# Kernel tuning notes

Measured on AMD Instinct MI355X. Metric: run time of the kernel, lower is better.

## Reference

```python
import jax, jax.numpy as jnp
import numpy as np

B, T, D, H = 4, 2048, 1024, 16
Dh = D // H          # 64 head dim
NF = Dh // 2         # 32 rotary frequencies


def setup_inputs() -> dict:
    key = jax.random.key(0)
    k0, k1, k2, k3 = jax.random.split(key, 4)
    x = jax.random.normal(k0, (B, T, D), dtype=jnp.float32)
    # 3D spatial coordinates per token, e.g. voxel positions
    coords = jax.random.uniform(k1, (B, T, 3), dtype=jnp.float32, minval=0.0, maxval=64.0)
    w_scale = 1.0 / np.sqrt(D)
    qkv_w = jax.random.normal(k2, (3 * D, D), dtype=jnp.float32) * w_scale
    qkv_b = jnp.zeros((3 * D,), dtype=jnp.float32)
    proj_w = jax.random.normal(k3, (D, D), dtype=jnp.float32) * w_scale
    proj_b = jnp.zeros((D,), dtype=jnp.float32)
    # mixed-axis rope: frequency f uses coordinate axis (f % 3), geometric period spacing within each axis group
    axes = (jnp.arange(NF) % 3).astype(jnp.int32)
    group = (jnp.arange(NF) // 3).astype(jnp.float32)
    n_per_axis = float(NF) / 3.0
    inv_freq = (10000.0 ** (-group / n_per_axis)).astype(jnp.float32)
    return {"x": x, "coords": coords, "qkv_w": qkv_w, "qkv_b": qkv_b,
            "proj_w": proj_w, "proj_b": proj_b, "inv_freq": inv_freq, "axes": axes}


def _apply_rope(t, sin, cos):
    # t: [B, H, T, Dh]; sin/cos: [B, 1, T, Dh//2]  (rotate-half convention)
    t1, t2 = jnp.split(t, 2, axis=-1)
    return jnp.concatenate([t1 * cos - t2 * sin, t1 * sin + t2 * cos], axis=-1)


def reference(x, coords, qkv_w, qkv_b, proj_w, proj_b, inv_freq, axes):
    b, t, d = x.shape
    # fused QKV projection
    qkv = (x @ qkv_w.T + qkv_b).reshape(b, t, 3, H, Dh)
    qkv = jnp.transpose(qkv, (2, 0, 3, 1, 4))     # [3, B, H, T, Dh]
    q, k, v = qkv[0], qkv[1], qkv[2]
    # vectorized per-sample rope from coords (replaces python loop over batch)
    ang = jnp.take(coords, axes, axis=-1) * inv_freq      # [B, T, NF]
    sin = jnp.sin(ang)[:, None]                            # [B, 1, T, NF]
    cos = jnp.cos(ang)[:, None]
    q = _apply_rope(q, sin, cos)
    k = _apply_rope(k, sin, cos)
    # standard scaling mode: single 1/sqrt(Dh) inside SDPA
    scale = 1.0 / np.sqrt(Dh)
    scores = jnp.einsum('bhqd,bhkd->bhqk', q, k) * scale
    attn = jax.nn.softmax(scores, axis=-1)
    out = jnp.einsum('bhqk,bhkd->bhqd', attn, v)           # [B, H, T, Dh]
    out = jnp.transpose(out, (0, 2, 1, 3)).reshape(b, t, d)
    return out @ proj_w.T + proj_b
```

## Files before the change

kernel.cpp:

```cpp
#include <hip/hip_runtime.h>
#include <hip/hip_bf16.h>

#define B_ 4
#define T_ 2048
#define D_ 1024
#define H_ 16
#define DH 64
#define NF 32
#define BH (B_*H_)
#define M_ROWS (B_*T_)

#define QSCALE 0.125f

using u16 = unsigned short;
using u32 = unsigned int;

typedef __bf16 bf16x8 __attribute__((ext_vector_type(8)));
typedef float  f32x4  __attribute__((ext_vector_type(4)));
typedef float  f32x16 __attribute__((ext_vector_type(16)));

__device__ __forceinline__ u16 f2bf(float f) {
  u32 u = __float_as_uint(f);
  u32 r = u + 0x7fffu + ((u >> 16) & 1u);
  return (u16)(r >> 16);
}
__device__ __forceinline__ u16 f2bf_hw(float f) {
  __bf16 h = (__bf16)f;
  return *(u16*)&h;
}
__device__ __forceinline__ u32 pack2(float lo, float hi) {
  return (u32)f2bf_hw(lo) | ((u32)f2bf_hw(hi) << 16);
}
__device__ __forceinline__ float bf2f(u16 h) {
  return __uint_as_float(((u32)h) << 16);
}

__device__ __forceinline__ void pl32swap(u32 a, u32 b, u32& x, u32& y) {
  x = a; y = b;
  asm("s_nop 1\n\t"
      "v_permlane32_swap_b32 %0, %1"
      : "+v"(x), "+v"(y));
}

__device__ __forceinline__ void gload_lds16(const void* g, void* l) {
  __builtin_amdgcn_global_load_lds((__attribute__((address_space(1))) void*)(g),
                                   (__attribute__((address_space(3))) void*)(l),
                                   16, 0, 0);
}

__global__ __launch_bounds__(256)
void cvt_kernel(const float* __restrict__ in, u16* __restrict__ out, int n8) {
  int idx = blockIdx.x * 256 + threadIdx.x;
  if (idx >= n8) return;
  const float4* p = (const float4*)in + (long)idx * 2;
  float4 a = p[0], b = p[1];
  u32 o0 = (u32)f2bf(a.x) | ((u32)f2bf(a.y) << 16);
  u32 o1 = (u32)f2bf(a.z) | ((u32)f2bf(a.w) << 16);
  u32 o2 = (u32)f2bf(b.x) | ((u32)f2bf(b.y) << 16);
  u32 o3 = (u32)f2bf(b.z) | ((u32)f2bf(b.w) << 16);
  ((uint4*)out)[idx] = make_uint4(o0, o1, o2, o3);
}

__global__ __launch_bounds__(256)
void sincos_kernel(const float* __restrict__ coords, const float* __restrict__ inv_freq,
                   const int* __restrict__ axes, float* __restrict__ sc) {
  int idx = blockIdx.x * 256 + threadIdx.x;
  if (idx >= B_ * T_ * NF) return;
  int f = idx & 31;
  long bt = idx >> 5;
  float c = coords[bt * 3 + axes[f]];
  float ang = c * inv_freq[f];
  sc[bt * 64 + f]      = sinf(ang);
  sc[bt * 64 + 32 + f] = cosf(ang);
}

__global__ __launch_bounds__(256, 2)
void gemm_qkv(const u16* __restrict__ A, const u16* __restrict__ Bt,
              const float* __restrict__ bias, const float* __restrict__ sc,
              u16* __restrict__ qr, u16* __restrict__ kr, u16* __restrict__ vt) {
  const int N = 3 * D_, K = D_;
  __shared__ u16 SMEM[128 * 64 * 2];
  u16* As = SMEM;
  u16* Bs = SMEM + 128 * 64;
  int nb = N >> 7;
  int bid = blockIdx.x;
  int nwg = gridDim.x;
  int cpx = nwg >> 3;
  bid = (bid & 7) * cpx + (bid >> 3);
  int bm = bid / nb, bn = bid % nb;
  long m0 = (long)bm << 7, n0 = (long)bn << 7;
  int tid = threadIdx.x;
  int lane = tid & 63, w = tid >> 6;
  int g = lane >> 4, lr = lane & 15;
  int wm = w >> 1, wn = w & 1;

  f32x4 acc[4][4] = {};

  for (int kt = 0; kt < K; kt += 64) {
    __syncthreads();
    #pragma unroll
    for (int j = 0; j < 4; ++j) {
      int ob = j * 4096 + tid * 16;
      int row = ob >> 7, col = (ob & 127) >> 1;
      u16* ldsA = As + j * 2048 + w * 512;
      u16* ldsB = Bs + j * 2048 + w * 512;
      gload_lds16(A + (m0 + row) * K + kt + col, ldsA);
      gload_lds16(Bt + (n0 + row) * K + kt + col, ldsB);
    }
    __syncthreads();
    #pragma unroll
    for (int kk = 0; kk < 2; ++kk) {
      bf16x8 af[4], bfr[4];
      #pragma unroll
      for (int i = 0; i < 4; ++i)
        af[i] = *(const bf16x8*)(As + (wm * 64 + i * 16 + lr) * 64 + kk * 32 + g * 8);
      #pragma unroll
      for (int i = 0; i < 4; ++i)
        bfr[i] = *(const bf16x8*)(Bs + (wn * 64 + i * 16 + lr) * 64 + kk * 32 + g * 8);
      #pragma unroll
      for (int mi = 0; mi < 4; ++mi)
        #pragma unroll
        for (int nj = 0; nj < 4; ++nj)
          acc[mi][nj] = __builtin_amdgcn_mfma_f32_16x16x32_bf16(af[mi], bfr[nj], acc[mi][nj], 0, 0, 0);
    }
  }

  int part = (int)(n0 >> 10);
  int b = (int)(m0 >> 11), t0 = (int)(m0 & 2047);
  float bv[4];
  #pragma unroll
  for (int nj = 0; nj < 4; ++nj)
    bv[nj] = bias[n0 + wn * 64 + nj * 16 + lr];

  if (part == 2) {
    int h0 = (int)((n0 & 1023) >> 6);
    u16* Vsm = SMEM;
    #pragma unroll
    for (int hsel = 0; hsel < 2; ++hsel) {
      __syncthreads();
      if (wn == hsel) {
        #pragma unroll
        for (int mi = 0; mi < 4; ++mi)
          #pragma unroll
          for (int i = 0; i < 4; ++i) {
            int lrow = wm * 64 + mi * 16 + g * 4 + i;
            #pragma unroll
            for (int nj = 0; nj < 4; ++nj)
              Vsm[lrow * 72 + nj * 16 + lr] = f2bf(acc[mi][nj][i] + bv[nj]);
          }
      }
      __syncthreads();
      int d = tid >> 2, tc = tid & 3;
      long obase = ((long)((b * 16 + h0 + hsel) * DH + d)) * T_ + t0 + tc * 32;
      #pragma unroll
      for (int c = 0; c < 4; ++c) {
        u32 o[4];
        #pragma unroll
        for (int j = 0; j < 4; ++j) {
          u16 lo = Vsm[(tc * 32 + c * 8 + 2 * j)     * 72 + d];
          u16 hi = Vsm[(tc * 32 + c * 8 + 2 * j + 1) * 72 + d];
          o[j] = (u32)lo | ((u32)hi << 16);
        }
        *(uint4*)(vt + obase + c * 8) = make_uint4(o[0], o[1], o[2], o[3]);
      }
    }
  } else {
    int h = ((int)(n0 & 1023) >> 6) + wn;
    u16* outp = part ? kr : qr;
    float fac = part ? 1.0f : QSCALE;
    #pragma unroll
    for (int mi = 0; mi < 4; ++mi) {
      #pragma unroll
      for (int i = 0; i < 4; ++i) {
        long row = m0 + wm * 64 + mi * 16 + g * 4 + i;
        long obase = ((long)((b * 16 + h)) * T_ + (row & 2047)) * 64;
        const float* scp = sc + row * 64;
        #pragma unroll
        for (int nj = 0; nj < 2; ++nj) {
          int d = nj * 16 + lr;
          float sn = scp[d], cs = scp[32 + d];
          float t1 = acc[mi][nj][i]     + bv[nj];
          float t2 = acc[mi][nj + 2][i] + bv[nj + 2];
          outp[obase + d]      = f2bf((t1 * cs - t2 * sn) * fac);
          outp[obase + 32 + d] = f2bf((t1 * sn + t2 * cs) * fac);
        }
      }
    }
  }
}

__global__ __launch_bounds__(256, 2)
void gemm_bt(const u16* __restrict__ A, const u16* __restrict__ Bt,
             const float* __restrict__ bias, float* __restrict__ Cout,
             int M, int N, int K) {
  __shared__ u16 As[128 * 64];
  __shared__ u16 Bs[128 * 64];
  int nb = N >> 7;
  int bid = blockIdx.x;
  int nwg = gridDim.x;
  if ((nwg & 7) == 0) {
    int c = nwg >> 3;
    bid = (bid & 7) * c + (bid >> 3);
  }
  int bm = bid / nb, bn = bid % nb;
  long m0 = (long)bm << 7, n0 = (long)bn << 7;
  int tid = threadIdx.x;
  int lane = tid & 63, w = tid >> 6;
  int g = lane >> 4, lr = lane & 15;
  int wm = w >> 1, wn = w & 1;

  f32x4 acc[4][4] = {};

  for (int kt = 0; kt < K; kt += 64) {
    __syncthreads();
    #pragma unroll
    for (int j = 0; j < 4; ++j) {
      int ob = j * 4096 + tid * 16;
      int row = ob >> 7, col = (ob & 127) >> 1;
      u16* ldsA = As + j * 2048 + w * 512;
      u16* ldsB = Bs + j * 2048 + w * 512;
      gload_lds16(A + (m0 + row) * K + kt + col, ldsA);
      gload_lds16(Bt + (n0 + row) * K + kt + col, ldsB);
    }
    __syncthreads();
    #pragma unroll
    for (int kk = 0; kk < 2; ++kk) {
      bf16x8 af[4], bfr[4];
      #pragma unroll
      for (int i = 0; i < 4; ++i)
        af[i] = *(const bf16x8*)(As + (wm * 64 + i * 16 + lr) * 64 + kk * 32 + g * 8);
      #pragma unroll
      for (int i = 0; i < 4; ++i)
        bfr[i] = *(const bf16x8*)(Bs + (wn * 64 + i * 16 + lr) * 64 + kk * 32 + g * 8);
      #pragma unroll
      for (int mi = 0; mi < 4; ++mi)
        #pragma unroll
        for (int nj = 0; nj < 4; ++nj)
          acc[mi][nj] = __builtin_amdgcn_mfma_f32_16x16x32_bf16(af[mi], bfr[nj], acc[mi][nj], 0, 0, 0);
    }
  }
  #pragma unroll
  for (int mi = 0; mi < 4; ++mi) {
    #pragma unroll
    for (int nj = 0; nj < 4; ++nj) {
      long col = n0 + wn * 64 + nj * 16 + lr;
      float bvv = bias[col];
      #pragma unroll
      for (int i = 0; i < 4; ++i) {
        long row = m0 + wm * 64 + mi * 16 + g * 4 + i;
        Cout[row * (long)N + col] = acc[mi][nj][i] + bvv;
      }
    }
  }
}

__global__ __launch_bounds__(256, 2)
void attn_kernel(const u16* __restrict__ Qr, const u16* __restrict__ Kr,
                 const u16* __restrict__ Vt, u16* __restrict__ Aout) {
  __shared__ u16 Ks[2][2][64 * 64];
  __shared__ u16 Vs[2][2][64 * 64];
  int wg = (blockIdx.x & 7) * 64 + (blockIdx.x >> 3);
  int bh = wg >> 3;
  int b = bh >> 4, h = bh & 15;
  int q0 = (wg & 7) << 8;
  int tid = threadIdx.x;
  int lane = tid & 63, w = tid >> 6;
  int l5 = lane & 31, hb = lane >> 5;

  const long tbase = (long)bh * T_;
  const long vbase = (long)bh * DH;
  const int qs = q0 + w * 64;

  bf16x8 bq0[4], bq1[4];
  #pragma unroll
  for (int s = 0; s < 4; ++s) {
    bq0[s] = *(const bf16x8*)(Qr + (tbase + qs + l5)      * DH + s * 16 + hb * 8);
    bq1[s] = *(const bf16x8*)(Qr + (tbase + qs + 32 + l5) * DH + s * 16 + hb * 8);
  }

  f32x16 oa00 = {}, oa01 = {};
  f32x16 oa10 = {}, oa11 = {};
  float ls0 = 0.f, ls1 = 0.f;

  const int sl = l5 & 7;

  auto STAGE = [&](int buf, int kb) {
    #pragma unroll
    for (int sub = 0; sub < 2; ++sub) {
      #pragma unroll
      for (int j = 0; j < 2; ++j) {
        int ob = j * 4096 + tid * 16;
        int row = ob >> 7;
        int c = ((ob >> 4) & 7) ^ (row & 7);
        u16* ldsK = Ks[buf][sub] + j * 2048 + w * 512;
        u16* ldsV = Vs[buf][sub] + j * 2048 + w * 512;
        gload_lds16(Kr + (tbase + kb + sub * 64 + row) * DH + c * 8, ldsK);
        gload_lds16(Vt + (vbase + row) * T_ + kb + sub * 64 + c * 8, ldsV);
      }
    }
  };

  STAGE(0, 0);
  asm volatile("s_waitcnt vmcnt(0)" ::: "memory");
  __builtin_amdgcn_s_barrier();
  __builtin_amdgcn_sched_barrier(0);

  int cur = 0;
  for (int kt = 0; kt < T_ / 128; ++kt) {
    if (kt + 1 < T_ / 128) STAGE(cur ^ 1, (kt + 1) * 128);

    #pragma unroll
    for (int h2 = 0; h2 < 2; ++h2) {
      const u16* kbuf = Ks[cur][h2];
      const u16* vbuf = Vs[cur][h2];

      f32x16 p00 = {}, p01 = {}, p10 = {}, p11 = {};
      #pragma unroll
      for (int s = 0; s < 4; ++s) {
        int c = ((2 * s + hb) ^ sl) * 8;
        bf16x8 ak0 = *(const bf16x8*)(kbuf + l5 * 64 + c);
        bf16x8 ak1 = *(const bf16x8*)(kbuf + (32 + l5) * 64 + c);
        p00 = __builtin_amdgcn_mfma_f32_32x32x16_bf16(ak0, bq0[s], p00, 0, 0, 0);
        p01 = __builtin_amdgcn_mfma_f32_32x32x16_bf16(ak1, bq0[s], p01, 0, 0, 0);
        p10 = __builtin_amdgcn_mfma_f32_32x32x16_bf16(ak0, bq1[s], p10, 0, 0, 0);
        p11 = __builtin_amdgcn_mfma_f32_32x32x16_bf16(ak1, bq1[s], p11, 0, 0, 0);
      }

      u32 pA0[8], pB0[8], pA1[8], pB1[8];
      #pragma unroll
      for (int r4 = 0; r4 < 4; ++r4) {
        float a0 = __expf(p00[4 * r4 + 0]), a1 = __expf(p00[4 * r4 + 1]);
        float a2 = __expf(p00[4 * r4 + 2]), a3 = __expf(p00[4 * r4 + 3]);
        ls0 += (a0 + a1) + (a2 + a3);
        pA0[r4] = pack2(a0, a1); pB0[r4] = pack2(a2, a3);
        float b0 = __expf(p01[4 * r4 + 0]), b1 = __expf(p01[4 * r4 + 1]);
        float b2 = __expf(p01[4 * r4 + 2]), b3 = __expf(p01[4 * r4 + 3]);
        ls0 += (b0 + b1) + (b2 + b3);
        pA0[4 + r4] = pack2(b0, b1); pB0[4 + r4] = pack2(b2, b3);
        float c0 = __expf(p10[4 * r4 + 0]), c1 = __expf(p10[4 * r4 + 1]);
        float c2 = __expf(p10[4 * r4 + 2]), c3 = __expf(p10[4 * r4 + 3]);
        ls1 += (c0 + c1) + (c2 + c3);
        pA1[r4] = pack2(c0, c1); pB1[r4] = pack2(c2, c3);
        float d0 = __expf(p11[4 * r4 + 0]), d1 = __expf(p11[4 * r4 + 1]);
        float d2 = __expf(p11[4 * r4 + 2]), d3 = __expf(p11[4 * r4 + 3]);
        ls1 += (d0 + d1) + (d2 + d3);
        pA1[4 + r4] = pack2(d0, d1); pB1[4 + r4] = pack2(d2, d3);
      }

      #pragma unroll
      for (int s2 = 0; s2 < 4; ++s2) {
        int c = ((2 * s2 + hb) ^ sl) * 8;
        bf16x8 av0 = *(const bf16x8*)(vbuf + l5 * 64 + c);
        bf16x8 av1 = *(const bf16x8*)(vbuf + (32 + l5) * 64 + c);
        u32 w0, w1, w2, w3;
        pl32swap(pA0[2 * s2], pA0[2 * s2 + 1], w0, w2);
        pl32swap(pB0[2 * s2], pB0[2 * s2 + 1], w1, w3);
        union { u32 u[4]; bf16x8 v; } bw0;
        bw0.u[0] = w0; bw0.u[1] = w1; bw0.u[2] = w2; bw0.u[3] = w3;
        oa00 = __builtin_amdgcn_mfma_f32_32x32x16_bf16(av0, bw0.v, oa00, 0, 0, 0);
        oa01 = __builtin_amdgcn_mfma_f32_32x32x16_bf16(av1, bw0.v, oa01, 0, 0, 0);
        pl32swap(pA1[2 * s2], pA1[2 * s2 + 1], w0, w2);
        pl32swap(pB1[2 * s2], pB1[2 * s2 + 1], w1, w3);
        union { u32 u[4]; bf16x8 v; } bw1;
        bw1.u[0] = w0; bw1.u[1] = w1; bw1.u[2] = w2; bw1.u[3] = w3;
        oa10 = __builtin_amdgcn_mfma_f32_32x32x16_bf16(av0, bw1.v, oa10, 0, 0, 0);
        oa11 = __builtin_amdgcn_mfma_f32_32x32x16_bf16(av1, bw1.v, oa11, 0, 0, 0);
      }
    }

    __builtin_amdgcn_sched_barrier(0);
    asm volatile("s_waitcnt vmcnt(0)" ::: "memory");
    __builtin_amdgcn_s_barrier();
    __builtin_amdgcn_sched_barrier(0);
    cur ^= 1;
  }

  ls0 += __shfl_xor(ls0, 32);
  ls1 += __shfl_xor(ls1, 32);
  float inv0 = 1.0f / ls0;
  float inv1 = 1.0f / ls1;
  long row0 = (long)b * T_ + qs + l5;
  u16* ob0 = Aout + row0 * D_ + h * DH;
  u16* ob1 = ob0 + 32 * D_;
  #pragma unroll
  for (int r4 = 0; r4 < 4; ++r4) {
    u32 w0 = pack2(oa00[4 * r4 + 0] * inv0, oa00[4 * r4 + 1] * inv0);
    u32 w1 = pack2(oa00[4 * r4 + 2] * inv0, oa00[4 * r4 + 3] * inv0);
    *(uint2*)(ob0 + r4 * 8 + hb * 4) = make_uint2(w0, w1);
    u32 w2 = pack2(oa01[4 * r4 + 0] * inv0, oa01[4 * r4 + 1] * inv0);
    u32 w3 = pack2(oa01[4 * r4 + 2] * inv0, oa01[4 * r4 + 3] * inv0);
    *(uint2*)(ob0 + 32 + r4 * 8 + hb * 4) = make_uint2(w2, w3);
    u32 w4 = pack2(oa10[4 * r4 + 0] * inv1, oa10[4 * r4 + 1] * inv1);
    u32 w5 = pack2(oa10[4 * r4 + 2] * inv1, oa10[4 * r4 + 3] * inv1);
    *(uint2*)(ob1 + r4 * 8 + hb * 4) = make_uint2(w4, w5);
    u32 w6 = pack2(oa11[4 * r4 + 0] * inv1, oa11[4 * r4 + 1] * inv1);
    u32 w7 = pack2(oa11[4 * r4 + 2] * inv1, oa11[4 * r4 + 3] * inv1);
    *(uint2*)(ob1 + 32 + r4 * 8 + hb * 4) = make_uint2(w6, w7);
  }
}

extern "C" void kernel_launch(void* const* d_in, const int* in_sizes, int n_in,
                              void* d_out, int out_size, void* d_ws, size_t ws_size,
                              hipStream_t stream) {
  const float* x        = (const float*)d_in[0];
  const float* coords   = (const float*)d_in[1];
  const float* qkv_w    = (const float*)d_in[2];
  const float* qkv_b    = (const float*)d_in[3];
  const float* proj_w   = (const float*)d_in[4];
  const float* proj_b   = (const float*)d_in[5];
  const float* inv_freq = (const float*)d_in[6];
  const int*   axes     = (const int*)d_in[7];
  float* out = (float*)d_out;

  char* ws = (char*)d_ws;
  size_t off = 0;
  auto alloc = [&](size_t bytes) -> char* {
    char* p = ws + off;
    off += (bytes + 255) & ~(size_t)255;
    return p;
  };
  u16*   xb     = (u16*)  alloc((size_t)M_ROWS * D_ * 2);
  u16*   wqkv   = (u16*)  alloc((size_t)3 * D_ * D_ * 2);
  u16*   wproj  = (u16*)  alloc((size_t)D_ * D_ * 2);
  float* sc     = (float*)alloc((size_t)M_ROWS * 64 * 4);
  u16*   qr     = (u16*)  alloc((size_t)BH * T_ * DH * 2);
  u16*   kr     = (u16*)  alloc((size_t)BH * T_ * DH * 2);
  u16*   vt     = (u16*)  alloc((size_t)BH * T_ * DH * 2);
  u16*   aout   = (u16*)  alloc((size_t)BH * T_ * DH * 2);

  cvt_kernel<<<(M_ROWS * D_ / 8 + 255) / 256, 256, 0, stream>>>(x, xb, M_ROWS * D_ / 8);
  cvt_kernel<<<(3 * D_ * D_ / 8 + 255) / 256, 256, 0, stream>>>(qkv_w, wqkv, 3 * D_ * D_ / 8);
  cvt_kernel<<<(D_ * D_ / 8 + 255) / 256, 256, 0, stream>>>(proj_w, wproj, D_ * D_ / 8);
  sincos_kernel<<<(B_ * T_ * NF + 255) / 256, 256, 0, stream>>>(coords, inv_freq, axes, sc);

  gemm_qkv<<<(M_ROWS / 128) * (3 * D_ / 128), 256, 0, stream>>>(xb, wqkv, qkv_b, sc,
                                                                qr, kr, vt);
  attn_kernel<<<512, 256, 0, stream>>>(qr, kr, vt, aout);
  gemm_bt<<<(M_ROWS / 128) * (D_ / 128), 256, 0, stream>>>(aout, wproj, proj_b, out,
                                                           M_ROWS, D_, D_);
}
```

Measured before the change: 203.8 us.

## Split attention KV range across two workgroups and merge partials in combine kernel

```diff
diff --git a/kernel.cpp b/kernel.cpp
--- a/kernel.cpp
+++ b/kernel.cpp
@@ -48,11 +48,9 @@
                                    16, 0, 0);
 }
 
-__global__ __launch_bounds__(256)
-void cvt_kernel(const float* __restrict__ in, u16* __restrict__ out, int n8) {
-  int idx = blockIdx.x * 256 + threadIdx.x;
-  if (idx >= n8) return;
-  const float4* p = (const float4*)in + (long)idx * 2;
+__device__ __forceinline__ void cvt8(const float* __restrict__ in,
+                                     u16* __restrict__ out, long idx) {
+  const float4* p = (const float4*)in + idx * 2;
   float4 a = p[0], b = p[1];
   u32 o0 = (u32)f2bf(a.x) | ((u32)f2bf(a.y) << 16);
   u32 o1 = (u32)f2bf(a.z) | ((u32)f2bf(a.w) << 16);
@@ -62,16 +60,31 @@
 }
 
 __global__ __launch_bounds__(256)
-void sincos_kernel(const float* __restrict__ coords, const float* __restrict__ inv_freq,
-                   const int* __restrict__ axes, float* __restrict__ sc) {
-  int idx = blockIdx.x * 256 + threadIdx.x;
-  if (idx >= B_ * T_ * NF) return;
-  int f = idx & 31;
-  long bt = idx >> 5;
-  float c = coords[bt * 3 + axes[f]];
-  float ang = c * inv_freq[f];
-  sc[bt * 64 + f]      = sinf(ang);
-  sc[bt * 64 + 32 + f] = cosf(ang);
+void prep_kernel(const float* __restrict__ x, u16* __restrict__ xb,
+                 const float* __restrict__ qkv_w, u16* __restrict__ wqkv,
+                 const float* __restrict__ proj_w, u16* __restrict__ wproj,
+                 const float* __restrict__ coords, const float* __restrict__ inv_freq,
+                 const int* __restrict__ axes, float* __restrict__ sc) {
+  long idx = (long)blockIdx.x * 256 + threadIdx.x;
+  const long n1 = (long)M_ROWS * D_ / 8;
+  const long n2 = n1 + 3L * D_ * D_ / 8;
+  const long n3 = n2 + (long)D_ * D_ / 8;
+  const long n4 = n3 + (long)B_ * T_ * NF;
+  if (idx < n1) {
+    cvt8(x, xb, idx);
+  } else if (idx < n2) {
+    cvt8(qkv_w, wqkv, idx - n1);
+  } else if (idx < n3) {
+    cvt8(proj_w, wproj, idx - n2);
+  } else if (idx < n4) {
+    long j = idx - n3;
+    int f = (int)(j & 31);
+    long bt = j >> 5;
+    float c = coords[bt * 3 + axes[f]];
+    float ang = c * inv_freq[f];
+    sc[bt * 64 + f]      = sinf(ang);
+    sc[bt * 64 + 32 + f] = cosf(ang);
+  }
 }
 
 __global__ __launch_bounds__(256, 2)
@@ -254,15 +267,19 @@
   }
 }
 
-__global__ __launch_bounds__(256, 2)
+__global__ __launch_bounds__(256, 4)
 void attn_kernel(const u16* __restrict__ Qr, const u16* __restrict__ Kr,
-                 const u16* __restrict__ Vt, u16* __restrict__ Aout) {
-  __shared__ u16 Ks[2][2][64 * 64];
-  __shared__ u16 Vs[2][2][64 * 64];
-  int wg = (blockIdx.x & 7) * 64 + (blockIdx.x >> 3);
-  int bh = wg >> 3;
+                 const u16* __restrict__ Vt, u16* __restrict__ P,
+                 float* __restrict__ L) {
+  __shared__ u16 Ks[2][64 * 64];
+  __shared__ u16 Vs[2][64 * 64];
+  int wg = (blockIdx.x & 7) * 128 + (blockIdx.x >> 3);
+  int bh = wg >> 4;
+  int sub = wg & 15;
+  int q0 = (sub >> 1) << 8;
+  int kv = sub & 1;
+  int kb0 = kv << 10;
   int b = bh >> 4, h = bh & 15;
-  int q0 = (wg & 7) << 8;
   int tid = threadIdx.x;
   int lane = tid & 63, w = tid >> 6;
   int l5 = lane & 31, hb = lane >> 5;
@@ -286,86 +303,80 @@
 
   auto STAGE = [&](int buf, int kb) {
     #pragma unroll
-    for (int sub = 0; sub < 2; ++sub) {
-      #pragma unroll
-      for (int j = 0; j < 2; ++j) {
-        int ob = j * 4096 + tid * 16;
-        int row = ob >> 7;
-        int c = ((ob >> 4) & 7) ^ (row & 7);
-        u16* ldsK = Ks[buf][sub] + j * 2048 + w * 512;
-        u16* ldsV = Vs[buf][sub] + j * 2048 + w * 512;
-        gload_lds16(Kr + (tbase + kb + sub * 64 + row) * DH + c * 8, ldsK);
-        gload_lds16(Vt + (vbase + row) * T_ + kb + sub * 64 + c * 8, ldsV);
-      }
+    for (int j = 0; j < 2; ++j) {
+      int ob = j * 4096 + tid * 16;
+      int row = ob >> 7;
+      int c = ((ob >> 4) & 7) ^ (row & 7);
+      u16* ldsK = Ks[buf] + j * 2048 + w * 512;
+      u16* ldsV = Vs[buf] + j * 2048 + w * 512;
+      gload_lds16(Kr + (tbase + kb + row) * DH + c * 8, ldsK);
+      gload_lds16(Vt + (vbase + row) * T_ + kb + c * 8, ldsV);
     }
   };
 
-  STAGE(0, 0);
+  STAGE(0, kb0);
   asm volatile("s_waitcnt vmcnt(0)" ::: "memory");
   __builtin_amdgcn_s_barrier();
   __builtin_amdgcn_sched_barrier(0);
 
   int cur = 0;
-  for (int kt = 0; kt < T_ / 128; ++kt) {
-    if (kt + 1 < T_ / 128) STAGE(cur ^ 1, (kt + 1) * 128);
-
-    #pragma unroll
-    for (int h2 = 0; h2 < 2; ++h2) {
-      const u16* kbuf = Ks[cur][h2];
-      const u16* vbuf = Vs[cur][h2];
-
-      f32x16 p00 = {}, p01 = {}, p10 = {}, p11 = {};
-      #pragma unroll
-      for (int s = 0; s < 4; ++s) {
-        int c = ((2 * s + hb) ^ sl) * 8;
-        bf16x8 ak0 = *(const bf16x8*)(kbuf + l5 * 64 + c);
-        bf16x8 ak1 = *(const bf16x8*)(kbuf + (32 + l5) * 64 + c);
-        p00 = __builtin_amdgcn_mfma_f32_32x32x16_bf16(ak0, bq0[s], p00, 0, 0, 0);
-        p01 = __builtin_amdgcn_mfma_f32_32x32x16_bf16(ak1, bq0[s], p01, 0, 0, 0);
-        p10 = __builtin_amdgcn_mfma_f32_32x32x16_bf16(ak0, bq1[s], p10, 0, 0, 0);
-        p11 = __builtin_amdgcn_mfma_f32_32x32x16_bf16(ak1, bq1[s], p11, 0, 0, 0);
-      }
-
-      u32 pA0[8], pB0[8], pA1[8], pB1[8];
-      #pragma unroll
-      for (int r4 = 0; r4 < 4; ++r4) {
-        float a0 = __expf(p00[4 * r4 + 0]), a1 = __expf(p00[4 * r4 + 1]);
-        float a2 = __expf(p00[4 * r4 + 2]), a3 = __expf(p00[4 * r4 + 3]);
-        ls0 += (a0 + a1) + (a2 + a3);
-        pA0[r4] = pack2(a0, a1); pB0[r4] = pack2(a2, a3);
-        float b0 = __expf(p01[4 * r4 + 0]), b1 = __expf(p01[4 * r4 + 1]);
-        float b2 = __expf(p01[4 * r4 + 2]), b3 = __expf(p01[4 * r4 + 3]);
-        ls0 += (b0 + b1) + (b2 + b3);
-        pA0[4 + r4] = pack2(b0, b1); pB0[4 + r4] = pack2(b2, b3);
-        float c0 = __expf(p10[4 * r4 + 0]), c1 = __expf(p10[4 * r4 + 1]);
-        float c2 = __expf(p10[4 * r4 + 2]), c3 = __expf(p10[4 * r4 + 3]);
-        ls1 += (c0 + c1) + (c2 + c3);
-        pA1[r4] = pack2(c0, c1); pB1[r4] = pack2(c2, c3);
-        float d0 = __expf(p11[4 * r4 + 0]), d1 = __expf(p11[4 * r4 + 1]);
-        float d2 = __expf(p11[4 * r4 + 2]), d3 = __expf(p11[4 * r4 + 3]);
-        ls1 += (d0 + d1) + (d2 + d3);
-        pA1[4 + r4] = pack2(d0, d1); pB1[4 + r4] = pack2(d2, d3);
-      }
-
-      #pragma unroll
-      for (int s2 = 0; s2 < 4; ++s2) {
-        int c = ((2 * s2 + hb) ^ sl) * 8;
-        bf16x8 av0 = *(const bf16x8*)(vbuf + l5 * 64 + c);
-        bf16x8 av1 = *(const bf16x8*)(vbuf + (32 + l5) * 64 + c);
-        u32 w0, w1, w2, w3;
-        pl32swap(pA0[2 * s2], pA0[2 * s2 + 1], w0, w2);
-        pl32swap(pB0[2 * s2], pB0[2 * s2 + 1], w1, w3);
-        union { u32 u[4]; bf16x8 v; } bw0;
-        bw0.u[0] = w0; bw0.u[1] = w1; bw0.u[2] = w2; bw0.u[3] = w3;
-        oa00 = __builtin_amdgcn_mfma_f32_32x32x16_bf16(av0, bw0.v, oa00, 0, 0, 0);
-        oa01 = __builtin_amdgcn_mfma_f32_32x32x16_bf16(av1, bw0.v, oa01, 0, 0, 0);
-        pl32swap(pA1[2 * s2], pA1[2 * s2 + 1], w0, w2);
-        pl32swap(pB1[2 * s2], pB1[2 * s2 + 1], w1, w3);
-        union { u32 u[4]; bf16x8 v; } bw1;
-        bw1.u[0] = w0; bw1.u[1] = w1; bw1.u[2] = w2; bw1.u[3] = w3;
-        oa10 = __builtin_amdgcn_mfma_f32_32x32x16_bf16(av0, bw1.v, oa10, 0, 0, 0);
-        oa11 = __builtin_amdgcn_mfma_f32_32x32x16_bf16(av1, bw1.v, oa11, 0, 0, 0);
-      }
+  for (int kt = 0; kt < 16; ++kt) {
+    if (kt + 1 < 16) STAGE(cur ^ 1, kb0 + (kt + 1) * 64);
+
+    const u16* kbuf = Ks[cur];
+    const u16* vbuf = Vs[cur];
+
+    f32x16 p00 = {}, p01 = {}, p10 = {}, p11 = {};
+    #pragma unroll
+    for (int s = 0; s < 4; ++s) {
+      int c = ((2 * s + hb) ^ sl) * 8;
+      bf16x8 ak0 = *(const bf16x8*)(kbuf + l5 * 64 + c);
+      bf16x8 ak1 = *(const bf16x8*)(kbuf + (32 + l5) * 64 + c);
+      p00 = __builtin_amdgcn_mfma_f32_32x32x16_bf16(ak0, bq0[s], p00, 0, 0, 0);
+      p01 = __builtin_amdgcn_mfma_f32_32x32x16_bf16(ak1, bq0[s], p01, 0, 0, 0);
+      p10 = __builtin_amdgcn_mfma_f32_32x32x16_bf16(ak0, bq1[s], p10, 0, 0, 0);
+      p11 = __builtin_amdgcn_mfma_f32_32x32x16_bf16(ak1, bq1[s], p11, 0, 0, 0);
+    }
+
+    u32 pA0[8], pB0[8], pA1[8], pB1[8];
+    #pragma unroll
+    for (int r4 = 0; r4 < 4; ++r4) {
+      float a0 = __expf(p00[4 * r4 + 0]), a1 = __expf(p00[4 * r4 + 1]);
+      float a2 = __expf(p00[4 * r4 + 2]), a3 = __expf(p00[4 * r4 + 3]);
+      ls0 += (a0 + a1) + (a2 + a3);
+      pA0[r4] = pack2(a0, a1); pB0[r4] = pack2(a2, a3);
+      float b0 = __expf(p01[4 * r4 + 0]), b1 = __expf(p01[4 * r4 + 1]);
+      float b2 = __expf(p01[4 * r4 + 2]), b3 = __expf(p01[4 * r4 + 3]);
+      ls0 += (b0 + b1) + (b2 + b3);
+      pA0[4 + r4] = pack2(b0, b1); pB0[4 + r4] = pack2(b2, b3);
+      float c0 = __expf(p10[4 * r4 + 0]), c1 = __expf(p10[4 * r4 + 1]);
+      float c2 = __expf(p10[4 * r4 + 2]), c3 = __expf(p10[4 * r4 + 3]);
+      ls1 += (c0 + c1) + (c2 + c3);
+      pA1[r4] = pack2(c0, c1); pB1[r4] = pack2(c2, c3);
+      float d0 = __expf(p11[4 * r4 + 0]), d1 = __expf(p11[4 * r4 + 1]);
+      float d2 = __expf(p11[4 * r4 + 2]), d3 = __expf(p11[4 * r4 + 3]);
+      ls1 += (d0 + d1) + (d2 + d3);
+      pA1[4 + r4] = pack2(d0, d1); pB1[4 + r4] = pack2(d2, d3);
+    }
+
+    #pragma unroll
+    for (int s2 = 0; s2 < 4; ++s2) {
+      int c = ((2 * s2 + hb) ^ sl) * 8;
+      bf16x8 av0 = *(const bf16x8*)(vbuf + l5 * 64 + c);
+      bf16x8 av1 = *(const bf16x8*)(vbuf + (32 + l5) * 64 + c);
+      u32 w0, w1, w2, w3;
+      pl32swap(pA0[2 * s2], pA0[2 * s2 + 1], w0, w2);
+      pl32swap(pB0[2 * s2], pB0[2 * s2 + 1], w1, w3);
+      union { u32 u[4]; bf16x8 v; } bw0;
+      bw0.u[0] = w0; bw0.u[1] = w1; bw0.u[2] = w2; bw0.u[3] = w3;
+      oa00 = __builtin_amdgcn_mfma_f32_32x32x16_bf16(av0, bw0.v, oa00, 0, 0, 0);
+      oa01 = __builtin_amdgcn_mfma_f32_32x32x16_bf16(av1, bw0.v, oa01, 0, 0, 0);
+      pl32swap(pA1[2 * s2], pA1[2 * s2 + 1], w0, w2);
+      pl32swap(pB1[2 * s2], pB1[2 * s2 + 1], w1, w3);
+      union { u32 u[4]; bf16x8 v; } bw1;
+      bw1.u[0] = w0; bw1.u[1] = w1; bw1.u[2] = w2; bw1.u[3] = w3;
+      oa10 = __builtin_amdgcn_mfma_f32_32x32x16_bf16(av0, bw1.v, oa10, 0, 0, 0);
+      oa11 = __builtin_amdgcn_mfma_f32_32x32x16_bf16(av1, bw1.v, oa11, 0, 0, 0);
     }
 
     __builtin_amdgcn_sched_barrier(0);
@@ -377,26 +388,59 @@
 
   ls0 += __shfl_xor(ls0, 32);
   ls1 += __shfl_xor(ls1, 32);
-  float inv0 = 1.0f / ls0;
-  float inv1 = 1.0f / ls1;
+  const long PS = (long)BH * T_ * DH;
+  u16* Pout = P + (long)kv * PS;
   long row0 = (long)b * T_ + qs + l5;
-  u16* ob0 = Aout + row0 * D_ + h * DH;
+  u16* ob0 = Pout + row0 * D_ + h * DH;
   u16* ob1 = ob0 + 32 * D_;
   #pragma unroll
   for (int r4 = 0; r4 < 4; ++r4) {
-    u32 w0 = pack2(oa00[4 * r4 + 0] * inv0, oa00[4 * r4 + 1] * inv0);
-    u32 w1 = pack2(oa00[4 * r4 + 2] * inv0, oa00[4 * r4 + 3] * inv0);
+    u32 w0 = pack2(oa00[4 * r4 + 0], oa00[4 * r4 + 1]);
+    u32 w1 = pack2(oa00[4 * r4 + 2], oa00[4 * r4 + 3]);
     *(uint2*)(ob0 + r4 * 8 + hb * 4) = make_uint2(w0, w1);
-    u32 w2 = pack2(oa01[4 * r4 + 0] * inv0, oa01[4 * r4 + 1] * inv0);
-    u32 w3 = pack2(oa01[4 * r4 + 2] * inv0, oa01[4 * r4 + 3] * inv0);
+    u32 w2 = pack2(oa01[4 * r4 + 0], oa01[4 * r4 + 1]);
+    u32 w3 = pack2(oa01[4 * r4 + 2], oa01[4 * r4 + 3]);
     *(uint2*)(ob0 + 32 + r4 * 8 + hb * 4) = make_uint2(w2, w3);
-    u32 w4 = pack2(oa10[4 * r4 + 0] * inv1, oa10[4 * r4 + 1] * inv1);
-    u32 w5 = pack2(oa10[4 * r4 + 2] * inv1, oa10[4 * r4 + 3] * inv1);
+    u32 w4 = pack2(oa10[4 * r4 + 0], oa10[4 * r4 + 1]);
+    u32 w5 = pack2(oa10[4 * r4 + 2], oa10[4 * r4 + 3]);
     *(uint2*)(ob1 + r4 * 8 + hb * 4) = make_uint2(w4, w5);
-    u32 w6 = pack2(oa11[4 * r4 + 0] * inv1, oa11[4 * r4 + 1] * inv1);
-    u32 w7 = pack2(oa11[4 * r4 + 2] * inv1, oa11[4 * r4 + 3] * inv1);
+    u32 w6 = pack2(oa11[4 * r4 + 0], oa11[4 * r4 + 1]);
+    u32 w7 = pack2(oa11[4 * r4 + 2], oa11[4 * r4 + 3]);
     *(uint2*)(ob1 + 32 + r4 * 8 + hb * 4) = make_uint2(w6, w7);
   }
+  if (hb == 0) {
+    float* lp = L + (long)kv * (BH * (long)T_) + ((long)bh << 11);
+    lp[qs + l5]      = ls0;
+    lp[qs + 32 + l5] = ls1;
+  }
+}
+
+__global__ __launch_bounds__(256)
+void combine_kernel(const u16* __restrict__ P, const float* __restrict__ L,
+                    u16* __restrict__ out) {
+  long idx = (long)blockIdx.x * 256 + threadIdx.x;
+  if (idx >= (long)M_ROWS * D_ / 8) return;
+  long e0 = idx << 3;
+  long row = e0 >> 10;
+  int col = (int)(e0 & 1023);
+  int h = col >> 6;
+  int b = (int)(row >> 11), t = (int)(row & 2047);
+  long pl = ((long)(b * 16 + h) << 11) + t;
+  const long PS = (long)BH * T_ * DH;
+  const long LS = (long)BH * T_;
+  float inv = 1.0f / (L[pl] + L[LS + pl]);
+  uint4 u0 = *(const uint4*)(P + e0);
+  uint4 u1 = *(const uint4*)(P + PS + e0);
+  u32 a[4] = {u0.x, u0.y, u0.z, u0.w};
+  u32 c[4] = {u1.x, u1.y, u1.z, u1.w};
+  u32 o[4];
+  #pragma unroll
+  for (int j = 0; j < 4; ++j) {
+    float lo = bf2f((u16)(a[j] & 0xffff)) + bf2f((u16)(c[j] & 0xffff));
+    float hi = bf2f((u16)(a[j] >> 16))    + bf2f((u16)(c[j] >> 16));
+    o[j] = pack2(lo * inv, hi * inv);
+  }
+  *(uint4*)(out + e0) = make_uint4(o[0], o[1], o[2], o[3]);
 }
 
 extern "C" void kernel_launch(void* const* d_in, const int* in_sizes, int n_in,
@@ -426,16 +470,16 @@
   u16*   qr     = (u16*)  alloc((size_t)BH * T_ * DH * 2);
   u16*   kr     = (u16*)  alloc((size_t)BH * T_ * DH * 2);
   u16*   vt     = (u16*)  alloc((size_t)BH * T_ * DH * 2);
-  u16*   aout   = (u16*)  alloc((size_t)BH * T_ * DH * 2);
-
-  cvt_kernel<<<(M_ROWS * D_ / 8 + 255) / 256, 256, 0, stream>>>(x, xb, M_ROWS * D_ / 8);
-  cvt_kernel<<<(3 * D_ * D_ / 8 + 255) / 256, 256, 0, stream>>>(qkv_w, wqkv, 3 * D_ * D_ / 8);
-  cvt_kernel<<<(D_ * D_ / 8 + 255) / 256, 256, 0, stream>>>(proj_w, wproj, D_ * D_ / 8);
-  sincos_kernel<<<(B_ * T_ * NF + 255) / 256, 256, 0, stream>>>(coords, inv_freq, axes, sc);
-
+  u16*   Pp     = (u16*)  alloc((size_t)2 * BH * T_ * DH * 2);
+  float* Lp     = (float*)alloc((size_t)2 * BH * T_ * 4);
+  u16*   aout   = xb;
+
+  prep_kernel<<<7168, 256, 0, stream>>>(x, xb, qkv_w, wqkv, proj_w, wproj,
+                                        coords, inv_freq, axes, sc);
   gemm_qkv<<<(M_ROWS / 128) * (3 * D_ / 128), 256, 0, stream>>>(xb, wqkv, qkv_b, sc,
                                                                 qr, kr, vt);
-  attn_kernel<<<512, 256, 0, stream>>>(qr, kr, vt, aout);
+  attn_kernel<<<1024, 256, 0, stream>>>(qr, kr, vt, Pp, Lp);
+  combine_kernel<<<(M_ROWS * D_ / 8 + 255) / 256, 256, 0, stream>>>(Pp, Lp, aout);
   gemm_bt<<<(M_ROWS / 128) * (D_ / 128), 256, 0, stream>>>(aout, wproj, proj_b, out,
                                                            M_ROWS, D_, D_);
 }
```

Result: slower. 613.2 us (+200.9%).
